# Kernel tuning notes

Hardware: AMD Instinct MI355X
Metric: run time of the kernel (lower is better)

Reference implementation:

```python
import jax, jax.numpy as jnp
import numpy as np

B, T, C, L = 256, 512, 256, 64
NEG = -1e30  # log-space 'zero'
BLANK = 0


def setup_inputs() -> dict:
    key = jax.random.key(0)
    k1, k2, k3, k4 = jax.random.split(key, 4)
    logits = jax.random.normal(k1, (B, T, C), dtype=jnp.float32)
    targets = jax.random.randint(k2, (B, L), 1, C)            # labels never equal blank (0)
    input_lengths = jax.random.randint(k3, (B,), T - 100, T + 1)
    target_lengths = jax.random.randint(k4, (B,), L // 2, L + 1)
    return dict(logits=logits, targets=targets,
                input_lengths=input_lengths, target_lengths=target_lengths)


def _ctc_loss(logits, targets, input_lengths, target_lengths):
    Bb, Tt, Cc = logits.shape
    Ll = targets.shape[1]
    S = 2 * Ll + 1  # extended label length (blanks interleaved)

    # fused log_softmax over vocab (original does permute then log_softmax; same math)
    logp = jax.nn.log_softmax(logits, axis=-1)  # [B,T,C]

    # extended target sequence: blank, y1, blank, y2, ..., blank
    ext = jnp.zeros((Bb, S), jnp.int32).at[:, 1::2].set(targets.astype(jnp.int32))
    # gather log-probs of extended labels for every timestep: [B,T,S]
    lp_ext = jnp.take_along_axis(logp, jnp.broadcast_to(ext[:, None, :], (Bb, Tt, S)), axis=2)

    # skip transition s-2 -> s allowed iff ext[s] != blank and ext[s] != ext[s-2]
    skip = jnp.zeros((Bb, S), bool).at[:, 2:].set(
        (ext[:, 2:] != BLANK) & (ext[:, 2:] != ext[:, :-2]))

    # alpha at t=0
    alpha0 = (jnp.full((Bb, S), NEG, dtype=logits.dtype)
              .at[:, 0].set(lp_ext[:, 0, 0])
              .at[:, 1].set(lp_ext[:, 0, 1]))

    neg1 = jnp.full((Bb, 1), NEG, dtype=logits.dtype)
    neg2 = jnp.full((Bb, 2), NEG, dtype=logits.dtype)

    def step(alpha, inputs):
        lp_t, t = inputs  # lp_t: [B,S]
        a1 = alpha
        a2 = jnp.concatenate([neg1, alpha[:, :-1]], axis=1)
        a3 = jnp.where(skip, jnp.concatenate([neg2, alpha[:, :-2]], axis=1), NEG)
        new = jnp.logaddexp(jnp.logaddexp(a1, a2), a3) + lp_t
        new = jnp.maximum(new, NEG)  # keep impossible paths bounded
        # freeze alpha for batch rows whose input sequence already ended
        alpha = jnp.where((t < input_lengths)[:, None], new, alpha)
        return alpha, None

    ts = jnp.arange(1, Tt)
    alphaT, _ = jax.lax.scan(step, alpha0, (jnp.swapaxes(lp_ext, 0, 1)[1:], ts))

    tl = target_lengths.astype(jnp.int32)
    a_last = jnp.take_along_axis(alphaT, (2 * tl)[:, None], axis=1)[:, 0]
    a_prev = jnp.take_along_axis(alphaT, (2 * tl - 1)[:, None], axis=1)[:, 0]
    loss = -jnp.logaddexp(a_last, a_prev)            # [B]
    loss = jnp.where(loss > 1e20, 0.0, loss)          # zero_infinity=True
    # reduction='mean': per-sample loss divided by target length, then batch mean
    return (loss / tl.astype(loss.dtype)).mean()


def reference(logits, targets, input_lengths, target_lengths):
    return _ctc_loss(logits, targets, input_lengths, target_lengths)
```

## Files before the change

### kernel.cpp

```cpp
#include <hip/hip_runtime.h>

#define B_ 256
#define T_ 512
#define C_ 256
#define L_ 64
#define S_ 129
#define TCH 64
#define NEG -1e30f
#define LOG2E 1.44269504f
#define LN2 0.69314718f

__device__ __forceinline__ unsigned short f2h(float f) {
    _Float16 h = (_Float16)f;
    return __builtin_bit_cast(unsigned short, h);
}
__device__ __forceinline__ float h2f(unsigned short u) {
    return (float)__builtin_bit_cast(_Float16, u);
}

__device__ __forceinline__ float shr1(float x, float fill) {
    int r = __builtin_amdgcn_update_dpp(__builtin_bit_cast(int, fill),
                                        __builtin_bit_cast(int, x),
                                        0x138, 0xF, 0xF, false);
    return __builtin_bit_cast(float, r);
}

__device__ __forceinline__ void ctc_step(float& a0, float& a1, float& a2,
                                         unsigned int q, bool skip) {
    const float lpb = h2f((unsigned short)(q & 0xffffu));
    const float lpo = h2f((unsigned short)(q >> 16));
    const float p = shr1(a1, NEG);
    const float m0 = fmaxf(a0, p), n0 = fminf(a0, p);
    const float a0n = m0 + __log2f(1.0f + exp2f(n0 - m0)) + lpb;
    const float c  = skip ? p : NEG;
    const float m1 = fmaxf(fmaxf(a1, a0), c);
    const float s1 = exp2f(a1 - m1) + exp2f(a0 - m1) + exp2f(c - m1);
    const float a1n = m1 + __log2f(s1) + lpo;
    const float m2 = fmaxf(a2, a1), n2 = fminf(a2, a1);
    const float a2n = m2 + __log2f(1.0f + exp2f(n2 - m2)) + lpb;
    a0 = a0n; a1 = a1n; a2 = a2n;
}

__global__ __launch_bounds__(576) void k_fused(const float* __restrict__ logits,
                                               const int* __restrict__ targets,
                                               const int* __restrict__ in_len,
                                               const int* __restrict__ tg_len,
                                               float* __restrict__ out) {
    const int b = blockIdx.x;
    const int w = threadIdx.x >> 6;
    const int l = threadIdx.x & 63;

    __shared__ unsigned int Gs[2][TCH][64];
    __shared__ int   tgt_sh[L_];
    __shared__ float alpha_sh[S_];

    if (threadIdx.x < L_) tgt_sh[threadIdx.x] = targets[(b << 6) + threadIdx.x];
    __syncthreads();

    const int len = in_len[b];
    float a0 = NEG, a1 = NEG, a2 = NEG;
    bool skip = false;
    if (w == 0) {
        const int tc = tgt_sh[l];
        const int tp = __shfl_up(tc, 1);
        skip = (l >= 1) && (tc != tp);
    }

    const size_t rowbase = (size_t)b * T_;

    for (int k = 0; k < 9; ++k) {
        if (w > 0 && k < 8) {
            const int tt0 = (w - 1) * 8;
            #pragma unroll
            for (int r = 0; r < 8; ++r) {
                const int tt = tt0 + r;
                const int t  = k * TCH + tt;
                const float4 v = ((const float4*)logits)[(rowbase + t) * 64 + l];
                const float yx = v.x * LOG2E, yy = v.y * LOG2E;
                const float yz = v.z * LOG2E, yw = v.w * LOG2E;
                float s = exp2f(yx) + exp2f(yy) + exp2f(yz) + exp2f(yw);
                #pragma unroll
                for (int off = 32; off; off >>= 1) s += __shfl_xor(s, off);
                const float lse2 = __log2f(s);
                const float lpb  = __shfl(yx, 0) - lse2;
                const float lv   = logits[(rowbase + t) * C_ + tgt_sh[l]] * LOG2E;
                const float lpo  = lv - lse2;
                Gs[k & 1][tt][l] = (unsigned int)f2h(lpb) | ((unsigned int)f2h(lpo) << 16);
            }
        }
        if (w == 0 && k >= 1) {
            const int base = (k - 1) * TCH;
            unsigned int q[TCH];
            #pragma unroll
            for (int tt = 0; tt < TCH; ++tt) q[tt] = Gs[(k - 1) & 1][tt][l];
            if (base == 0) {
                a0 = (l == 0) ? h2f((unsigned short)(q[0] & 0xffffu)) : NEG;
                a1 = (l == 0) ? h2f((unsigned short)(q[0] >> 16))     : NEG;
                a2 = NEG;
            }
            #pragma unroll
            for (int tt = 0; tt < TCH; ++tt) {
                const int t = base + tt;
                if (t >= 1 && t < len)
                    ctc_step(a0, a1, a2, q[tt], skip);
            }
        }
        __syncthreads();
    }

    if (w == 0) {
        alpha_sh[2 * l]     = a0;
        alpha_sh[2 * l + 1] = a1;
        if (l == 63) alpha_sh[128] = a2;
    }
    __syncthreads();
    if (threadIdx.x == 0) {
        const int tl = tg_len[b];
        const float al = alpha_sh[2 * tl];
        const float ap = alpha_sh[2 * tl - 1];
        const float m  = fmaxf(al, ap);
        float loss = -LN2 * (m + __log2f(exp2f(al - m) + exp2f(ap - m)));
        if (loss > 1e20f) loss = 0.0f;
        atomicAdd(out, loss / (float)tl * (1.0f / (float)B_));
    }
}

extern "C" void kernel_launch(void* const* d_in, const int* in_sizes, int n_in,
                              void* d_out, int out_size, void* d_ws, size_t ws_size,
                              hipStream_t stream) {
    const float* logits  = (const float*)d_in[0];
    const int*   targets = (const int*)d_in[1];
    const int*   in_len  = (const int*)d_in[2];
    const int*   tg_len  = (const int*)d_in[3];
    float*       out     = (float*)d_out;

    hipMemsetAsync(d_out, 0, sizeof(float), stream);
    k_fused<<<B_, 576, 0, stream>>>(logits, targets, in_len, tg_len, out);
}
```

Before: 227.0 us.

## Batch logit loads, use DPP wave reduction, and prioritize the recurrence wave

Producer waves now issue all eight row loads and target gathers up front before computing, so more memory requests are in flight at once. The shuffle-based wave sum becomes a DPP row/broadcast reduction with a readlane, and the blank logit is taken via readfirstlane. The recurrence wave raises its scheduling priority and reads shared memory in double-buffered groups of eight instead of one 64-entry register array. This aims to shorten the serial alpha recurrence and hide load latency, at the cost of more producer registers, which may lower occupancy.

```diff
diff --git a/kernel.cpp b/kernel.cpp
--- a/kernel.cpp
+++ b/kernel.cpp
@@ -23,6 +23,24 @@
                                         __builtin_bit_cast(int, x),
                                         0x138, 0xF, 0xF, false);
     return __builtin_bit_cast(float, r);
+}
+
+__device__ __forceinline__ float wave_sum(float x) {
+#define DPPADD(ctrl)                                                          \
+    {                                                                         \
+        int _t = __builtin_amdgcn_update_dpp(0, __builtin_bit_cast(int, x),   \
+                                             (ctrl), 0xF, 0xF, true);         \
+        x += __builtin_bit_cast(float, _t);                                   \
+    }
+    DPPADD(0x111)
+    DPPADD(0x112)
+    DPPADD(0x114)
+    DPPADD(0x118)
+    DPPADD(0x142)
+    DPPADD(0x143)
+#undef DPPADD
+    return __builtin_bit_cast(float,
+        __builtin_amdgcn_readlane(__builtin_bit_cast(int, x), 63));
 }
 
 __device__ __forceinline__ void ctc_step(float& a0, float& a1, float& a2,
@@ -64,45 +82,65 @@
         const int tc = tgt_sh[l];
         const int tp = __shfl_up(tc, 1);
         skip = (l >= 1) && (tc != tp);
+        __builtin_amdgcn_s_setprio(1);
     }
+    const int mytgt = tgt_sh[l];
 
     const size_t rowbase = (size_t)b * T_;
 
     for (int k = 0; k < 9; ++k) {
         if (w > 0 && k < 8) {
             const int tt0 = (w - 1) * 8;
+            float4 v[8];
+            float  lv[8];
+            #pragma unroll
+            for (int r = 0; r < 8; ++r) {
+                const int t = k * TCH + tt0 + r;
+                v[r]  = ((const float4*)logits)[(rowbase + t) * 64 + l];
+                lv[r] = logits[(rowbase + t) * C_ + mytgt];
+            }
             #pragma unroll
             for (int r = 0; r < 8; ++r) {
                 const int tt = tt0 + r;
-                const int t  = k * TCH + tt;
-                const float4 v = ((const float4*)logits)[(rowbase + t) * 64 + l];
-                const float yx = v.x * LOG2E, yy = v.y * LOG2E;
-                const float yz = v.z * LOG2E, yw = v.w * LOG2E;
+                const float yx = v[r].x * LOG2E, yy = v[r].y * LOG2E;
+                const float yz = v[r].z * LOG2E, yw = v[r].w * LOG2E;
                 float s = exp2f(yx) + exp2f(yy) + exp2f(yz) + exp2f(yw);
-                #pragma unroll
-                for (int off = 32; off; off >>= 1) s += __shfl_xor(s, off);
-                const float lse2 = __log2f(s);
-                const float lpb  = __shfl(yx, 0) - lse2;
-                const float lv   = logits[(rowbase + t) * C_ + tgt_sh[l]] * LOG2E;
-                const float lpo  = lv - lse2;
-                Gs[k & 1][tt][l] = (unsigned int)f2h(lpb) | ((unsigned int)f2h(lpo) << 16);
+                const float stot = wave_sum(s);
+                const float lse2 = __log2f(stot);
+                const float lpb  = __builtin_bit_cast(float,
+                    __builtin_amdgcn_readfirstlane(__builtin_bit_cast(int, yx))) - lse2;
+                const float lpo  = lv[r] * LOG2E - lse2;
+                Gs[k & 1][tt][l] = (unsigned int)f2h(lpb)
+                                 | ((unsigned int)f2h(lpo) << 16);
             }
         }
         if (w == 0 && k >= 1) {
+            const int kb = (k - 1) & 1;
             const int base = (k - 1) * TCH;
-            unsigned int q[TCH];
+            unsigned int qa[8], qb[8];
             #pragma unroll
-            for (int tt = 0; tt < TCH; ++tt) q[tt] = Gs[(k - 1) & 1][tt][l];
+            for (int j = 0; j < 8; ++j) qa[j] = Gs[kb][j][l];
             if (base == 0) {
-                a0 = (l == 0) ? h2f((unsigned short)(q[0] & 0xffffu)) : NEG;
-                a1 = (l == 0) ? h2f((unsigned short)(q[0] >> 16))     : NEG;
+                a0 = (l == 0) ? h2f((unsigned short)(qa[0] & 0xffffu)) : NEG;
+                a1 = (l == 0) ? h2f((unsigned short)(qa[0] >> 16))     : NEG;
                 a2 = NEG;
             }
-            #pragma unroll
-            for (int tt = 0; tt < TCH; ++tt) {
-                const int t = base + tt;
-                if (t >= 1 && t < len)
-                    ctc_step(a0, a1, a2, q[tt], skip);
+            for (int g = 0; g < 8; ++g) {
+                if (g < 7) {
+                    #pragma unroll
+                    for (int j = 0; j < 8; ++j)
+                        qb[j] = Gs[kb][(g + 1) * 8 + j][l];
+                }
+                #pragma unroll
+                for (int j = 0; j < 8; ++j) {
+                    const int t = base + g * 8 + j;
+                    if (t >= 1 && t < len)
+                        ctc_step(a0, a1, a2, qa[j], skip);
+                }
+                if (g < 7) {
+                    #pragma unroll
+                    for (int j = 0; j < 8; ++j) qa[j] = qb[j];
+                }
             }
         }
         __syncthreads();
```

Result: no change. 230.6 us (+1.6%).
